# Kernel tuning notes

Hardware: AMD Instinct MI355X
Metric: run time of the kernel (lower is better)

Reference implementation:

```python
import jax, jax.numpy as jnp
import numpy as np

B, NQ, NK, H, DV = 4, 128, 1024, 256, 256
NEG_INF = -1e6


def setup_inputs() -> dict:
    key = jax.random.key(0)
    ks = jax.random.split(key, 7)
    return {
        "queries": jax.random.normal(ks[0], (B, NQ, H), dtype=jnp.float32),
        "keys": jax.random.normal(ks[1], (B, NK, H), dtype=jnp.float32),
        "values": jax.random.normal(ks[2], (B, NK, DV), dtype=jnp.float32),
        "valid_lens": jax.random.randint(ks[3], (B,), 1, NK + 1, dtype=jnp.int32),
        "Wq": jax.random.normal(ks[4], (H, H), dtype=jnp.float32) * (1.0 / np.sqrt(H)),
        "Wk": jax.random.normal(ks[5], (H, H), dtype=jnp.float32) * (1.0 / np.sqrt(H)),
        "wv": jax.random.normal(ks[6], (H,), dtype=jnp.float32) * (1.0 / np.sqrt(H)),
    }


def reference(queries, keys, values, valid_lens, Wq, Wk, wv):
    # Project queries and keys: nn.Linear(x) = x @ W.T
    q = jnp.einsum('bqd,hd->bqh', queries, Wq)  # (B,NQ,H)
    k = jnp.einsum('bkd,hd->bkh', keys, Wk)     # (B,NK,H)
    # Broadcasted add -> tanh -> scalar projection: (B,NQ,NK,H) intermediate
    features = jnp.tanh(q[:, :, None, :] + k[:, None, :, :])
    scores = jnp.einsum('bqkh,h->bqk', features, wv)  # (B,NQ,NK)
    # masked_softmax over the key axis: positions >= valid_len get -1e6
    mask = jnp.arange(scores.shape[-1])[None, None, :] < valid_lens[:, None, None]
    scores = jnp.where(mask, scores, NEG_INF)
    attn = jax.nn.softmax(scores, axis=-1)  # (B,NQ,NK)
    # dropout p=0.0 (identity). Weighted sum over values.
    return jnp.einsum('bqk,bkv->bqv', attn, values)  # (B,NQ,DV)
```

## Files before the change

kernel.cpp:

```cpp
#include <hip/hip_runtime.h>
#include <hip/hip_bf16.h>
#include <cmath>

#define B 4
#define NQ 128
#define NK 1024
#define HD 256
#define DV 256

__global__ __launch_bounds__(256) void proj_exp(
    const float* __restrict__ Xq, const float* __restrict__ Xk,
    const float* __restrict__ Wq, const float* __restrict__ Wk,
    float* __restrict__ Eq, float* __restrict__ Ek)
{
    const int z = blockIdx.z;
    if (z == 0 && blockIdx.x >= (B * NQ) / 64) return;
    const float* __restrict__ X = z ? Xk : Xq;
    const float* __restrict__ W = z ? Wk : Wq;
    float* __restrict__ E = z ? Ek : Eq;

    __shared__ float sX[64][68];
    __shared__ float sW[64][68];
    const int tid = threadIdx.x;
    const int bm = blockIdx.x * 64;
    const int bh = blockIdx.y * 64;
    const int ty = tid >> 4, tx = tid & 15;
    const int lr = tid >> 2;
    const int lc = (tid & 3) << 4;

    float acc[4][4] = {};

    for (int ks = 0; ks < HD; ks += 64) {
        #pragma unroll
        for (int j = 0; j < 4; ++j) {
            const int d = lc + j * 4;
            float4 xv = *(const float4*)&X[(size_t)(bm + lr) * HD + ks + d];
            float4 wm = *(const float4*)&W[(size_t)(bh + lr) * HD + ks + d];
            sX[d + 0][lr] = xv.x; sX[d + 1][lr] = xv.y;
            sX[d + 2][lr] = xv.z; sX[d + 3][lr] = xv.w;
            sW[d + 0][lr] = wm.x; sW[d + 1][lr] = wm.y;
            sW[d + 2][lr] = wm.z; sW[d + 3][lr] = wm.w;
        }
        __syncthreads();
        #pragma unroll 8
        for (int kk = 0; kk < 64; ++kk) {
            float4 a4 = *(const float4*)&sX[kk][ty * 4];
            float4 b4 = *(const float4*)&sW[kk][tx * 4];
            float av[4] = {a4.x, a4.y, a4.z, a4.w};
            float bv[4] = {b4.x, b4.y, b4.z, b4.w};
            #pragma unroll
            for (int i = 0; i < 4; ++i)
                #pragma unroll
                for (int j = 0; j < 4; ++j)
                    acc[i][j] = fmaf(av[i], bv[j], acc[i][j]);
        }
        __syncthreads();
    }

    const int m0 = bm + ty * 4;
    const int h0 = bh + tx * 4;
    #pragma unroll
    for (int i = 0; i < 4; ++i) {
        float4 e4 = {__expf(2.0f * acc[i][0]), __expf(2.0f * acc[i][1]),
                     __expf(2.0f * acc[i][2]), __expf(2.0f * acc[i][3])};
        *(float4*)&E[(size_t)(m0 + i) * HD + h0] = e4;
    }
}

__device__ __forceinline__ void quad_acc(float& acc, float4 q, float4 k, float4 w)
{
    float d0 = fmaf(q.x, k.x, 1.0f);
    float d1 = fmaf(q.y, k.y, 1.0f);
    float d2 = fmaf(q.z, k.z, 1.0f);
    float d3 = fmaf(q.w, k.w, 1.0f);
    float n01 = fmaf(w.x, d1, w.y * d0);
    float d01 = d0 * d1;
    float n23 = fmaf(w.z, d3, w.w * d2);
    float d23 = d2 * d3;
    float n  = fmaf(n01, d23, n23 * d01);
    float dd = d01 * d23;
    acc = fmaf(n, __builtin_amdgcn_rcpf(dd), acc);
}

__global__ __launch_bounds__(256) void scores_kernel(
    const float* __restrict__ Eq, const float* __restrict__ Ek,
    const float* __restrict__ wv, float* __restrict__ scores)
{
    __shared__ float s_q[32][68];
    __shared__ float s_k[32][68];
    __shared__ float s_w[64];
    const int tid = threadIdx.x;
    const int kb = blockIdx.x * 32;
    const int qb = blockIdx.y * 32;
    const int b  = blockIdx.z;
    const int ty = tid >> 4, tx = tid & 15;

    float a00 = 0.f, a01 = 0.f, a10 = 0.f, a11 = 0.f;
    const size_t qbase = ((size_t)b * NQ + qb) * HD;
    const size_t kbase = ((size_t)b * NK + kb) * HD;

    const int srow = tid >> 3;
    const int scol = (tid & 7) << 3;

    for (int hc = 0; hc < HD; hc += 64) {
        {
            const float* qp = &Eq[qbase + (size_t)srow * HD + hc + scol];
            const float* kp = &Ek[kbase + (size_t)srow * HD + hc + scol];
            float4 q0 = *(const float4*)qp;
            float4 q1 = *(const float4*)(qp + 4);
            float4 k0 = *(const float4*)kp;
            float4 k1 = *(const float4*)(kp + 4);
            *(float4*)&s_q[srow][scol]     = q0;
            *(float4*)&s_q[srow][scol + 4] = q1;
            *(float4*)&s_k[srow][scol]     = k0;
            *(float4*)&s_k[srow][scol + 4] = k1;
            if (tid < 16) {
                float4 w = *(const float4*)&wv[hc + tid * 4];
                s_w[tid * 4 + 0] = -2.0f * w.x;
                s_w[tid * 4 + 1] = -2.0f * w.y;
                s_w[tid * 4 + 2] = -2.0f * w.z;
                s_w[tid * 4 + 3] = -2.0f * w.w;
            }
        }
        __syncthreads();
        #pragma unroll
        for (int i = 0; i < 16; ++i) {
            const int h4 = i << 2;
            const float4 W4 = *(const float4*)&s_w[h4];
            const float4 Q0 = *(const float4*)&s_q[ty][h4];
            const float4 Q1 = *(const float4*)&s_q[ty + 16][h4];
            const float4 K0 = *(const float4*)&s_k[tx][h4];
            const float4 K1 = *(const float4*)&s_k[tx + 16][h4];
            quad_acc(a00, Q0, K0, W4);
            quad_acc(a01, Q0, K1, W4);
            quad_acc(a10, Q1, K0, W4);
            quad_acc(a11, Q1, K1, W4);
        }
        __syncthreads();
    }

    const size_t r0 = ((size_t)b * NQ + qb + ty) * NK;
    const size_t r1 = ((size_t)b * NQ + qb + ty + 16) * NK;
    scores[r0 + kb + tx]      = a00;
    scores[r0 + kb + tx + 16] = a01;
    scores[r1 + kb + tx]      = a10;
    scores[r1 + kb + tx + 16] = a11;
}

__global__ __launch_bounds__(256) void softmax_kernel(float* __restrict__ scores,
                                                      const int* __restrict__ valid_lens)
{
    const int row = blockIdx.x;
    const int b = row >> 7;
    const int valid = valid_lens[b];
    float* s = scores + (size_t)row * NK;
    const int tid = threadIdx.x;

    float4 v = *(const float4*)&s[tid * 4];
    float x[4] = {v.x, v.y, v.z, v.w};
    #pragma unroll
    for (int j = 0; j < 4; ++j) {
        const int k = tid * 4 + j;
        if (k >= valid) x[j] = -1e6f;
    }
    float m = fmaxf(fmaxf(x[0], x[1]), fmaxf(x[2], x[3]));
    #pragma unroll
    for (int off = 32; off >= 1; off >>= 1)
        m = fmaxf(m, __shfl_xor(m, off));

    __shared__ float redm[4], reds[4];
    const int wid = tid >> 6, lane = tid & 63;
    if (lane == 0) redm[wid] = m;
    __syncthreads();
    m = fmaxf(fmaxf(redm[0], redm[1]), fmaxf(redm[2], redm[3]));

    float p[4], psum = 0.f;
    #pragma unroll
    for (int j = 0; j < 4; ++j) { p[j] = __expf(x[j] - m); psum += p[j]; }
    #pragma unroll
    for (int off = 32; off >= 1; off >>= 1)
        psum += __shfl_xor(psum, off);
    if (lane == 0) reds[wid] = psum;
    __syncthreads();
    const float total = reds[0] + reds[1] + reds[2] + reds[3];
    const float inv = 1.0f / total;

    float4 o = {p[0] * inv, p[1] * inv, p[2] * inv, p[3] * inv};
    *(float4*)&s[tid * 4] = o;
}

__global__ __launch_bounds__(256) void pv_partial(const float* __restrict__ attn,
                                                  const float* __restrict__ values,
                                                  float* __restrict__ partial)
{
    __shared__ float s_a[16][128];
    const int tid = threadIdx.x;
    const int ks = blockIdx.x, qg = blockIdx.y, b = blockIdx.z;
    const int q0 = qg * 16;
    const int k0 = ks * 128;

    #pragma unroll
    for (int f0 = 0; f0 < 2; ++f0) {
        const int f = tid + f0 * 256;
        const int row = f >> 5;
        const int col = (f & 31) << 2;
        *(float4*)&s_a[row][col] =
            *(const float4*)&attn[((size_t)b * NQ + q0 + row) * NK + k0 + col];
    }
    __syncthreads();

    float acc[16] = {};
    #pragma unroll 8
    for (int k = 0; k < 128; ++k) {
        const float va = values[((size_t)b * NK + k0 + k) * DV + tid];
        #pragma unroll
        for (int q = 0; q < 16; ++q)
            acc[q] = fmaf(s_a[q][k], va, acc[q]);
    }

    const size_t pbase = (size_t)ks * (B * NQ * DV) + ((size_t)b * NQ + q0) * DV + tid;
    #pragma unroll
    for (int q = 0; q < 16; ++q)
        partial[pbase + (size_t)q * DV] = acc[q];
}

__global__ __launch_bounds__(256) void reduce_pv(const float* __restrict__ partial,
                                                 float* __restrict__ out)
{
    const int i = blockIdx.x * 256 + threadIdx.x;
    float s = 0.f;
    #pragma unroll
    for (int p = 0; p < 8; ++p) s += partial[(size_t)p * (B * NQ * DV) + i];
    out[i] = s;
}

extern "C" void kernel_launch(void* const* d_in, const int* in_sizes, int n_in,
                              void* d_out, int out_size, void* d_ws, size_t ws_size,
                              hipStream_t stream) {
    const float* queries    = (const float*)d_in[0];
    const float* keys       = (const float*)d_in[1];
    const float* values     = (const float*)d_in[2];
    const int*   valid_lens = (const int*)  d_in[3];
    const float* Wq         = (const float*)d_in[4];
    const float* Wk         = (const float*)d_in[5];
    const float* wv         = (const float*)d_in[6];
    float* out = (float*)d_out;

    float* ws      = (float*)d_ws;
    float* Eq      = ws;
    float* Ek      = Eq + (size_t)B * NQ * HD;
    float* scores  = Ek + (size_t)B * NK * HD;
    float* partial = scores + (size_t)B * NQ * NK;

    proj_exp<<<dim3((B * NK) / 64, HD / 64, 2), 256, 0, stream>>>(
        queries, keys, Wq, Wk, Eq, Ek);
    scores_kernel<<<dim3(NK / 32, NQ / 32, B), 256, 0, stream>>>(Eq, Ek, wv, scores);
    softmax_kernel<<<dim3(B * NQ), 256, 0, stream>>>(scores, valid_lens);
    pv_partial<<<dim3(8, NQ / 16, B), 256, 0, stream>>>(scores, values, partial);
    reduce_pv<<<dim3((B * NQ * DV) / 256), 256, 0, stream>>>(partial, out);
}
```

Before: 129.1 us.

## Fuse all attention stages into one persistent kernel with grid barriers

Replaces the five separate kernel launches with one persistent 256-block kernel that runs key projection, split-K query projection, scores, masked softmax, PV partials and the final reduction in sequence, separated by atomic-counter grid barriers. The query projection is split eight ways along the inner dimension into a partial buffer so all 256 blocks have work, and a later phase reduces it and applies the exp. The aim is to remove per-launch overhead and the inter-kernel gaps. In exchange it adds several grid-wide spin barriers and a memset, and it relies on all 256 blocks being resident at once without a cooperative launch.

```diff
diff --git a/kernel.cpp b/kernel.cpp
--- a/kernel.cpp
+++ b/kernel.cpp
@@ -1,5 +1,4 @@
 #include <hip/hip_runtime.h>
-#include <hip/hip_bf16.h>
 #include <cmath>
 
 #define B 4
@@ -7,45 +6,120 @@
 #define NK 1024
 #define HD 256
 #define DV 256
-
-__global__ __launch_bounds__(256) void proj_exp(
-    const float* __restrict__ Xq, const float* __restrict__ Xk,
+#define NBLK 256
+#define NTHR 256
+
+union SMem {
+    struct { float sX[64][68]; float sW[64][68]; } proj;
+    struct { float s_q[32][68]; float s_k[32][68]; float s_w[64]; } sc;
+    struct { float s_a[16][128]; } pv;
+    struct { float redm[4]; float reds[4]; } sm;
+};
+
+__device__ __forceinline__ void grid_sync(unsigned* counter, unsigned* gen)
+{
+    __syncthreads();
+    if (threadIdx.x == 0) {
+        __threadfence();
+        unsigned g = __atomic_load_n(gen, __ATOMIC_RELAXED);
+        if (__atomic_fetch_add(counter, 1u, __ATOMIC_ACQ_REL) == NBLK - 1u) {
+            __atomic_store_n(counter, 0u, __ATOMIC_RELAXED);
+            __atomic_fetch_add(gen, 1u, __ATOMIC_RELEASE);
+        } else {
+            while (__atomic_load_n(gen, __ATOMIC_ACQUIRE) == g)
+                __builtin_amdgcn_s_sleep(2);
+        }
+        __threadfence();
+    }
+    __syncthreads();
+}
+
+__global__ __launch_bounds__(NTHR) void mega_attn(
+    const float* __restrict__ queries, const float* __restrict__ keys,
+    const float* __restrict__ values, const int* __restrict__ valid_lens,
     const float* __restrict__ Wq, const float* __restrict__ Wk,
-    float* __restrict__ Eq, float* __restrict__ Ek)
+    const float* __restrict__ wv, float* __restrict__ out,
+    float* __restrict__ Eq, float* __restrict__ Ek,
+    float* __restrict__ Qpart, float* __restrict__ scores,
+    float* __restrict__ partial, unsigned* __restrict__ bar)
 {
-    const int z = blockIdx.z;
-    if (z == 0 && blockIdx.x >= (B * NQ) / 64) return;
-    const float* __restrict__ X = z ? Xk : Xq;
-    const float* __restrict__ W = z ? Wk : Wq;
-    float* __restrict__ E = z ? Ek : Eq;
-
-    __shared__ float sX[64][68];
-    __shared__ float sW[64][68];
+    unsigned* counter = bar;
+    unsigned* gen     = bar + 1;
+    __shared__ SMem sm_;
     const int tid = threadIdx.x;
-    const int bm = blockIdx.x * 64;
-    const int bh = blockIdx.y * 64;
+    const int bid = blockIdx.x;
     const int ty = tid >> 4, tx = tid & 15;
-    const int lr = tid >> 2;
-    const int lc = (tid & 3) << 4;
-
-    float acc[4][4] = {};
-
-    for (int ks = 0; ks < HD; ks += 64) {
-        #pragma unroll
-        for (int j = 0; j < 4; ++j) {
-            const int d = lc + j * 4;
-            float4 xv = *(const float4*)&X[(size_t)(bm + lr) * HD + ks + d];
-            float4 wm = *(const float4*)&W[(size_t)(bh + lr) * HD + ks + d];
-            sX[d + 0][lr] = xv.x; sX[d + 1][lr] = xv.y;
-            sX[d + 2][lr] = xv.z; sX[d + 3][lr] = xv.w;
-            sW[d + 0][lr] = wm.x; sW[d + 1][lr] = wm.y;
-            sW[d + 2][lr] = wm.z; sW[d + 3][lr] = wm.w;
-        }
-        __syncthreads();
+
+    {
+        const int bm = (bid >> 2) * 64;
+        const int bh = (bid & 3) * 64;
+        const int lr = tid >> 2;
+        const int lc = (tid & 3) << 4;
+        float acc[4][4] = {};
+        for (int ks = 0; ks < HD; ks += 64) {
+            #pragma unroll
+            for (int j = 0; j < 4; ++j) {
+                const int d = lc + j * 4;
+                float4 xv = *(const float4*)&keys[(size_t)(bm + lr) * HD + ks + d];
+                float4 wm = *(const float4*)&Wk [(size_t)(bh + lr) * HD + ks + d];
+                sm_.proj.sX[d + 0][lr] = xv.x; sm_.proj.sX[d + 1][lr] = xv.y;
+                sm_.proj.sX[d + 2][lr] = xv.z; sm_.proj.sX[d + 3][lr] = xv.w;
+                sm_.proj.sW[d + 0][lr] = wm.x; sm_.proj.sW[d + 1][lr] = wm.y;
+                sm_.proj.sW[d + 2][lr] = wm.z; sm_.proj.sW[d + 3][lr] = wm.w;
+            }
+            __syncthreads();
+            #pragma unroll 8
+            for (int kk = 0; kk < 64; ++kk) {
+                float4 a4 = *(const float4*)&sm_.proj.sX[kk][ty * 4];
+                float4 b4 = *(const float4*)&sm_.proj.sW[kk][tx * 4];
+                float av[4] = {a4.x, a4.y, a4.z, a4.w};
+                float bv[4] = {b4.x, b4.y, b4.z, b4.w};
+                #pragma unroll
+                for (int i = 0; i < 4; ++i)
+                    #pragma unroll
+                    for (int j = 0; j < 4; ++j)
+                        acc[i][j] = fmaf(av[i], bv[j], acc[i][j]);
+            }
+            __syncthreads();
+        }
+        const int m0 = bm + ty * 4, h0 = bh + tx * 4;
+        #pragma unroll
+        for (int i = 0; i < 4; ++i) {
+            float4 e4 = {__expf(2.0f * acc[i][0]), __expf(2.0f * acc[i][1]),
+                         __expf(2.0f * acc[i][2]), __expf(2.0f * acc[i][3])};
+            *(float4*)&Ek[(size_t)(m0 + i) * HD + h0] = e4;
+        }
+    }
+
+    {
+        const int s  = bid & 7;
+        const int tq = bid >> 3;
+        const int bm = (tq >> 2) * 64;
+        const int bh = (tq & 3) * 64;
+        const int k0 = s * 32;
+        const int lr  = tid >> 2;
+        const int lc2 = (tid & 3) * 8;
+        __syncthreads();
+        {
+            float4 xa = *(const float4*)&queries[(size_t)(bm + lr) * HD + k0 + lc2];
+            float4 xb = *(const float4*)&queries[(size_t)(bm + lr) * HD + k0 + lc2 + 4];
+            float4 wa = *(const float4*)&Wq[(size_t)(bh + lr) * HD + k0 + lc2];
+            float4 wb = *(const float4*)&Wq[(size_t)(bh + lr) * HD + k0 + lc2 + 4];
+            sm_.proj.sX[lc2 + 0][lr] = xa.x; sm_.proj.sX[lc2 + 1][lr] = xa.y;
+            sm_.proj.sX[lc2 + 2][lr] = xa.z; sm_.proj.sX[lc2 + 3][lr] = xa.w;
+            sm_.proj.sX[lc2 + 4][lr] = xb.x; sm_.proj.sX[lc2 + 5][lr] = xb.y;
+            sm_.proj.sX[lc2 + 6][lr] = xb.z; sm_.proj.sX[lc2 + 7][lr] = xb.w;
+            sm_.proj.sW[lc2 + 0][lr] = wa.x; sm_.proj.sW[lc2 + 1][lr] = wa.y;
+            sm_.proj.sW[lc2 + 2][lr] = wa.z; sm_.proj.sW[lc2 + 3][lr] = wa.w;
+            sm_.proj.sW[lc2 + 4][lr] = wb.x; sm_.proj.sW[lc2 + 5][lr] = wb.y;
+            sm_.proj.sW[lc2 + 6][lr] = wb.z; sm_.proj.sW[lc2 + 7][lr] = wb.w;
+        }
+        __syncthreads();
+        float acc[4][4] = {};
         #pragma unroll 8
-        for (int kk = 0; kk < 64; ++kk) {
-            float4 a4 = *(const float4*)&sX[kk][ty * 4];
-            float4 b4 = *(const float4*)&sW[kk][tx * 4];
+        for (int kk = 0; kk < 32; ++kk) {
+            float4 a4 = *(const float4*)&sm_.proj.sX[kk][ty * 4];
+            float4 b4 = *(const float4*)&sm_.proj.sW[kk][tx * 4];
             float av[4] = {a4.x, a4.y, a4.z, a4.w};
             float bv[4] = {b4.x, b4.y, b4.z, b4.w};
             #pragma unroll
@@ -54,184 +128,181 @@
                 for (int j = 0; j < 4; ++j)
                     acc[i][j] = fmaf(av[i], bv[j], acc[i][j]);
         }
-        __syncthreads();
-    }
-
-    const int m0 = bm + ty * 4;
-    const int h0 = bh + tx * 4;
-    #pragma unroll
-    for (int i = 0; i < 4; ++i) {
-        float4 e4 = {__expf(2.0f * acc[i][0]), __expf(2.0f * acc[i][1]),
-                     __expf(2.0f * acc[i][2]), __expf(2.0f * acc[i][3])};
-        *(float4*)&E[(size_t)(m0 + i) * HD + h0] = e4;
-    }
-}
-
-__device__ __forceinline__ void quad_acc(float& acc, float4 q, float4 k, float4 w)
-{
-    float d0 = fmaf(q.x, k.x, 1.0f);
-    float d1 = fmaf(q.y, k.y, 1.0f);
-    float d2 = fmaf(q.z, k.z, 1.0f);
-    float d3 = fmaf(q.w, k.w, 1.0f);
-    float n01 = fmaf(w.x, d1, w.y * d0);
-    float d01 = d0 * d1;
-    float n23 = fmaf(w.z, d3, w.w * d2);
-    float d23 = d2 * d3;
-    float n  = fmaf(n01, d23, n23 * d01);
-    float dd = d01 * d23;
-    acc = fmaf(n, __builtin_amdgcn_rcpf(dd), acc);
-}
-
-__global__ __launch_bounds__(256) void scores_kernel(
-    const float* __restrict__ Eq, const float* __restrict__ Ek,
-    const float* __restrict__ wv, float* __restrict__ scores)
-{
-    __shared__ float s_q[32][68];
-    __shared__ float s_k[32][68];
-    __shared__ float s_w[64];
-    const int tid = threadIdx.x;
-    const int kb = blockIdx.x * 32;
-    const int qb = blockIdx.y * 32;
-    const int b  = blockIdx.z;
-    const int ty = tid >> 4, tx = tid & 15;
-
-    float a00 = 0.f, a01 = 0.f, a10 = 0.f, a11 = 0.f;
-    const size_t qbase = ((size_t)b * NQ + qb) * HD;
-    const size_t kbase = ((size_t)b * NK + kb) * HD;
-
-    const int srow = tid >> 3;
-    const int scol = (tid & 7) << 3;
-
-    for (int hc = 0; hc < HD; hc += 64) {
-        {
-            const float* qp = &Eq[qbase + (size_t)srow * HD + hc + scol];
-            const float* kp = &Ek[kbase + (size_t)srow * HD + hc + scol];
-            float4 q0 = *(const float4*)qp;
-            float4 q1 = *(const float4*)(qp + 4);
-            float4 k0 = *(const float4*)kp;
-            float4 k1 = *(const float4*)(kp + 4);
-            *(float4*)&s_q[srow][scol]     = q0;
-            *(float4*)&s_q[srow][scol + 4] = q1;
-            *(float4*)&s_k[srow][scol]     = k0;
-            *(float4*)&s_k[srow][scol + 4] = k1;
-            if (tid < 16) {
-                float4 w = *(const float4*)&wv[hc + tid * 4];
-                s_w[tid * 4 + 0] = -2.0f * w.x;
-                s_w[tid * 4 + 1] = -2.0f * w.y;
-                s_w[tid * 4 + 2] = -2.0f * w.z;
-                s_w[tid * 4 + 3] = -2.0f * w.w;
+        float* qp = &Qpart[((size_t)(s * 32 + tq)) * 64 * 64];
+        #pragma unroll
+        for (int i = 0; i < 4; ++i) {
+            float4 p4 = {acc[i][0], acc[i][1], acc[i][2], acc[i][3]};
+            *(float4*)&qp[(ty * 4 + i) * 64 + tx * 4] = p4;
+        }
+    }
+    grid_sync(counter, gen);
+
+    {
+        #pragma unroll
+        for (int rep = 0; rep < 2; ++rep) {
+            const int q = bid * 2 + rep;
+            const int h = tid;
+            const int tq = (q >> 6) * 4 + (h >> 6);
+            const int qm = q & 63, hm = h & 63;
+            float ssum = 0.f;
+            #pragma unroll
+            for (int s2 = 0; s2 < 8; ++s2)
+                ssum += Qpart[(((size_t)(s2 * 32 + tq)) * 64 + qm) * 64 + hm];
+            Eq[(size_t)q * HD + h] = __expf(2.0f * ssum);
+        }
+    }
+    grid_sync(counter, gen);
+
+    for (int rep = 0; rep < 2; ++rep) {
+        const int tile = bid + rep * NBLK;
+        const int kb = (tile & 31) * 32;
+        const int qb = ((tile >> 5) & 3) * 32;
+        const int b  = tile >> 7;
+        float a00 = 0.f, a01 = 0.f, a10 = 0.f, a11 = 0.f;
+        const size_t qbase = ((size_t)b * NQ + qb) * HD;
+        const size_t kbase = ((size_t)b * NK + kb) * HD;
+        const int srow = tid >> 3;
+        const int scol = (tid & 7) << 3;
+        __syncthreads();
+        for (int hc = 0; hc < HD; hc += 64) {
+            {
+                const float* qp = &Eq[qbase + (size_t)srow * HD + hc + scol];
+                const float* kp = &Ek[kbase + (size_t)srow * HD + hc + scol];
+                float4 q0 = *(const float4*)qp;
+                float4 q1 = *(const float4*)(qp + 4);
+                float4 k0 = *(const float4*)kp;
+                float4 k1 = *(const float4*)(kp + 4);
+                *(float4*)&sm_.sc.s_q[srow][scol]     = q0;
+                *(float4*)&sm_.sc.s_q[srow][scol + 4] = q1;
+                *(float4*)&sm_.sc.s_k[srow][scol]     = k0;
+                *(float4*)&sm_.sc.s_k[srow][scol + 4] = k1;
+                if (tid < 16) {
+                    float4 w = *(const float4*)&wv[hc + tid * 4];
+                    sm_.sc.s_w[tid * 4 + 0] = -2.0f * w.x;
+                    sm_.sc.s_w[tid * 4 + 1] = -2.0f * w.y;
+                    sm_.sc.s_w[tid * 4 + 2] = -2.0f * w.z;
+                    sm_.sc.s_w[tid * 4 + 3] = -2.0f * w.w;
+                }
             }
-        }
-        __syncthreads();
-        #pragma unroll
-        for (int i = 0; i < 16; ++i) {
-            const int h4 = i << 2;
-            const float4 W4 = *(const float4*)&s_w[h4];
-            const float4 Q0 = *(const float4*)&s_q[ty][h4];
-            const float4 Q1 = *(const float4*)&s_q[ty + 16][h4];
-            const float4 K0 = *(const float4*)&s_k[tx][h4];
-            const float4 K1 = *(const float4*)&s_k[tx + 16][h4];
-            quad_acc(a00, Q0, K0, W4);
-            quad_acc(a01, Q0, K1, W4);
-            quad_acc(a10, Q1, K0, W4);
-            quad_acc(a11, Q1, K1, W4);
-        }
-        __syncthreads();
-    }
-
-    const size_t r0 = ((size_t)b * NQ + qb + ty) * NK;
-    const size_t r1 = ((size_t)b * NQ + qb + ty + 16) * NK;
-    scores[r0 + kb + tx]      = a00;
-    scores[r0 + kb + tx + 16] = a01;
-    scores[r1 + kb + tx]      = a10;
-    scores[r1 + kb + tx + 16] = a11;
-}
-
-__global__ __launch_bounds__(256) void softmax_kernel(float* __restrict__ scores,
-                                                      const int* __restrict__ valid_lens)
-{
-    const int row = blockIdx.x;
-    const int b = row >> 7;
-    const int valid = valid_lens[b];
-    float* s = scores + (size_t)row * NK;
-    const int tid = threadIdx.x;
-
-    float4 v = *(const float4*)&s[tid * 4];
-    float x[4] = {v.x, v.y, v.z, v.w};
-    #pragma unroll
-    for (int j = 0; j < 4; ++j) {
-        const int k = tid * 4 + j;
-        if (k >= valid) x[j] = -1e6f;
-    }
-    float m = fmaxf(fmaxf(x[0], x[1]), fmaxf(x[2], x[3]));
-    #pragma unroll
-    for (int off = 32; off >= 1; off >>= 1)
-        m = fmaxf(m, __shfl_xor(m, off));
-
-    __shared__ float redm[4], reds[4];
-    const int wid = tid >> 6, lane = tid & 63;
-    if (lane == 0) redm[wid] = m;
-    __syncthreads();
-    m = fmaxf(fmaxf(redm[0], redm[1]), fmaxf(redm[2], redm[3]));
-
-    float p[4], psum = 0.f;
-    #pragma unroll
-    for (int j = 0; j < 4; ++j) { p[j] = __expf(x[j] - m); psum += p[j]; }
-    #pragma unroll
-    for (int off = 32; off >= 1; off >>= 1)
-        psum += __shfl_xor(psum, off);
-    if (lane == 0) reds[wid] = psum;
-    __syncthreads();
-    const float total = reds[0] + reds[1] + reds[2] + reds[3];
-    const float inv = 1.0f / total;
-
-    float4 o = {p[0] * inv, p[1] * inv, p[2] * inv, p[3] * inv};
-    *(float4*)&s[tid * 4] = o;
-}
-
-__global__ __launch_bounds__(256) void pv_partial(const float* __restrict__ attn,
-                                                  const float* __restrict__ values,
-                                                  float* __restrict__ partial)
-{
-    __shared__ float s_a[16][128];
-    const int tid = threadIdx.x;
-    const int ks = blockIdx.x, qg = blockIdx.y, b = blockIdx.z;
-    const int q0 = qg * 16;
-    const int k0 = ks * 128;
-
-    #pragma unroll
-    for (int f0 = 0; f0 < 2; ++f0) {
-        const int f = tid + f0 * 256;
-        const int row = f >> 5;
-        const int col = (f & 31) << 2;
-        *(float4*)&s_a[row][col] =
-            *(const float4*)&attn[((size_t)b * NQ + q0 + row) * NK + k0 + col];
-    }
-    __syncthreads();
-
-    float acc[16] = {};
-    #pragma unroll 8
-    for (int k = 0; k < 128; ++k) {
-        const float va = values[((size_t)b * NK + k0 + k) * DV + tid];
+            __syncthreads();
+            #pragma unroll
+            for (int i = 0; i < 16; ++i) {
+                const int h4 = i << 2;
+                const float4 W4 = *(const float4*)&sm_.sc.s_w[h4];
+                const float4 Q0 = *(const float4*)&sm_.sc.s_q[ty][h4];
+                const float4 Q1 = *(const float4*)&sm_.sc.s_q[ty + 16][h4];
+                const float4 K0 = *(const float4*)&sm_.sc.s_k[tx][h4];
+                const float4 K1 = *(const float4*)&sm_.sc.s_k[tx + 16][h4];
+                #pragma unroll
+                for (int pair = 0; pair < 4; ++pair) {
+                    const float4* Qp = (pair < 2) ? &Q0 : &Q1;
+                    const float4* Kp = (pair & 1) ? &K1 : &K0;
+                    float d0 = fmaf(Qp->x, Kp->x, 1.0f);
+                    float d1 = fmaf(Qp->y, Kp->y, 1.0f);
+                    float d2 = fmaf(Qp->z, Kp->z, 1.0f);
+                    float d3 = fmaf(Qp->w, Kp->w, 1.0f);
+                    float n01 = fmaf(W4.x, d1, W4.y * d0);
+                    float d01 = d0 * d1;
+                    float n23 = fmaf(W4.z, d3, W4.w * d2);
+                    float d23 = d2 * d3;
+                    float n  = fmaf(n01, d23, n23 * d01);
+                    float dd = d01 * d23;
+                    float r  = fmaf(n, __builtin_amdgcn_rcpf(dd), 0.0f);
+                    if (pair == 0) a00 += r;
+                    else if (pair == 1) a01 += r;
+                    else if (pair == 2) a10 += r;
+                    else a11 += r;
+                }
+            }
+            __syncthreads();
+        }
+        const size_t r0 = ((size_t)b * NQ + qb + ty) * NK;
+        const size_t r1 = ((size_t)b * NQ + qb + ty + 16) * NK;
+        scores[r0 + kb + tx]      = a00;
+        scores[r0 + kb + tx + 16] = a01;
+        scores[r1 + kb + tx]      = a10;
+        scores[r1 + kb + tx + 16] = a11;
+    }
+    grid_sync(counter, gen);
+
+    for (int rep = 0; rep < 2; ++rep) {
+        const int row = bid * 2 + rep;
+        const int b = row >> 7;
+        const int valid = valid_lens[b];
+        float* s = scores + (size_t)row * NK;
+        float4 v = *(const float4*)&s[tid * 4];
+        float x[4] = {v.x, v.y, v.z, v.w};
+        #pragma unroll
+        for (int j = 0; j < 4; ++j) {
+            const int k = tid * 4 + j;
+            if (k >= valid) x[j] = -1e6f;
+        }
+        float m = fmaxf(fmaxf(x[0], x[1]), fmaxf(x[2], x[3]));
+        #pragma unroll
+        for (int off = 32; off >= 1; off >>= 1)
+            m = fmaxf(m, __shfl_xor(m, off));
+        const int wid = tid >> 6, lane = tid & 63;
+        if (lane == 0) sm_.sm.redm[wid] = m;
+        __syncthreads();
+        m = fmaxf(fmaxf(sm_.sm.redm[0], sm_.sm.redm[1]),
+                  fmaxf(sm_.sm.redm[2], sm_.sm.redm[3]));
+        float p[4], psum = 0.f;
+        #pragma unroll
+        for (int j = 0; j < 4; ++j) { p[j] = __expf(x[j] - m); psum += p[j]; }
+        #pragma unroll
+        for (int off = 32; off >= 1; off >>= 1)
+            psum += __shfl_xor(psum, off);
+        if (lane == 0) sm_.sm.reds[wid] = psum;
+        __syncthreads();
+        const float total = sm_.sm.reds[0] + sm_.sm.reds[1] +
+                            sm_.sm.reds[2] + sm_.sm.reds[3];
+        const float inv = 1.0f / total;
+        float4 o = {p[0] * inv, p[1] * inv, p[2] * inv, p[3] * inv};
+        *(float4*)&s[tid * 4] = o;
+        __syncthreads();
+    }
+    grid_sync(counter, gen);
+
+    {
+        const int ks = bid & 7, qg = (bid >> 3) & 7, b = bid >> 6;
+        const int q0 = qg * 16;
+        const int k0 = ks * 128;
+        #pragma unroll
+        for (int f0 = 0; f0 < 2; ++f0) {
+            const int f = tid + f0 * 256;
+            const int row = f >> 5;
+            const int col = (f & 31) << 2;
+            *(float4*)&sm_.pv.s_a[row][col] =
+                *(const float4*)&scores[((size_t)b * NQ + q0 + row) * NK + k0 + col];
+        }
+        __syncthreads();
+        float acc[16] = {};
+        #pragma unroll 8
+        for (int k = 0; k < 128; ++k) {
+            const float va = values[((size_t)b * NK + k0 + k) * DV + tid];
+            #pragma unroll
+            for (int q = 0; q < 16; ++q)
+                acc[q] = fmaf(sm_.pv.s_a[q][k], va, acc[q]);
+        }
+        const size_t pbase = (size_t)ks * (B * NQ * DV) +
+                             ((size_t)b * NQ + q0) * DV + tid;
         #pragma unroll
         for (int q = 0; q < 16; ++q)
-            acc[q] = fmaf(s_a[q][k], va, acc[q]);
-    }
-
-    const size_t pbase = (size_t)ks * (B * NQ * DV) + ((size_t)b * NQ + q0) * DV + tid;
-    #pragma unroll
-    for (int q = 0; q < 16; ++q)
-        partial[pbase + (size_t)q * DV] = acc[q];
-}
-
-__global__ __launch_bounds__(256) void reduce_pv(const float* __restrict__ partial,
-                                                 float* __restrict__ out)
-{
-    const int i = blockIdx.x * 256 + threadIdx.x;
-    float s = 0.f;
-    #pragma unroll
-    for (int p = 0; p < 8; ++p) s += partial[(size_t)p * (B * NQ * DV) + i];
-    out[i] = s;
+            partial[pbase + (size_t)q * DV] = acc[q];
+    }
+    grid_sync(counter, gen);
+
+    {
+        #pragma unroll
+        for (int rep = 0; rep < 2; ++rep) {
+            const int i = bid * 512 + rep * 256 + tid;
+            float ssum = 0.f;
+            #pragma unroll
+            for (int p = 0; p < 8; ++p)
+                ssum += partial[(size_t)p * (B * NQ * DV) + i];
+            out[i] = ssum;
+        }
+    }
 }
 
 extern "C" void kernel_launch(void* const* d_in, const int* in_sizes, int n_in,
@@ -249,13 +320,14 @@
     float* ws      = (float*)d_ws;
     float* Eq      = ws;
     float* Ek      = Eq + (size_t)B * NQ * HD;
-    float* scores  = Ek + (size_t)B * NK * HD;
+    float* Qpart   = Ek + (size_t)B * NK * HD;
+    float* scores  = Qpart + (size_t)8 * 32 * 64 * 64;
     float* partial = scores + (size_t)B * NQ * NK;
-
-    proj_exp<<<dim3((B * NK) / 64, HD / 64, 2), 256, 0, stream>>>(
-        queries, keys, Wq, Wk, Eq, Ek);
-    scores_kernel<<<dim3(NK / 32, NQ / 32, B), 256, 0, stream>>>(Eq, Ek, wv, scores);
-    softmax_kernel<<<dim3(B * NQ), 256, 0, stream>>>(scores, valid_lens);
-    pv_partial<<<dim3(8, NQ / 16, B), 256, 0, stream>>>(scores, values, partial);
-    reduce_pv<<<dim3((B * NQ * DV) / 256), 256, 0, stream>>>(partial, out);
+    unsigned* bar  = (unsigned*)(partial + (size_t)8 * B * NQ * DV);
+
+    hipMemsetAsync(bar, 0, 2 * sizeof(unsigned), stream);
+
+    mega_attn<<<dim3(NBLK), dim3(NTHR), 0, stream>>>(
+        queries, keys, values, valid_lens, Wq, Wk, wv, out,
+        Eq, Ek, Qpart, scores, partial, bar);
 }
```

Result: slower. 327.0 us (+153.2%).
